# Kernel tuning notes

Measured on AMD Instinct MI355X. Metric: run time of the kernel, lower is better.

Reference implementation:

```python
import jax, jax.numpy as jnp
import numpy as np

B, N, E = 64, 2048, 32768          # graphs, nodes/graph, edges/graph
DIM = 64
RATIO = 0.8
K1 = int(np.ceil(RATIO * N))        # 1639 nodes/graph after pool1
K2 = int(np.ceil(RATIO * K1))       # 1312 nodes/graph after pool2
NUM_CLASSES = 6


def gcn_conv(x, W, b, src, dst, valid, n):
    # GCNConv with self-loops: out = D^-1/2 (A+I) D^-1/2 (x W) + b
    xw = x @ W                                          # [n, DIM]
    deg = jnp.zeros(n, x.dtype).at[dst].add(valid) + 1.0  # in-degree incl. self-loop
    norm = valid * jax.lax.rsqrt(deg[src] * deg[dst])      # per-edge norm (0 for masked)
    agg = jnp.zeros_like(xw).at[dst].add(xw[src] * norm[:, None])
    return agg + xw / deg[:, None] + b                  # self-loop term has norm 1/deg


def topk_pool(x, p, n_graphs, n_per, k):
    # PyG TopKPooling: score = tanh(x.p/||p||); keep top-k per graph; gate x by score
    score = jnp.tanh((x @ p) / jnp.linalg.norm(p))       # [n_graphs*n_per]
    vals, idx = jax.lax.top_k(score.reshape(n_graphs, n_per), k)  # [n_graphs, k]
    xg = x.reshape(n_graphs, n_per, -1)
    sel = jnp.take_along_axis(xg, idx[..., None], axis=1)          # [n_graphs, k, DIM]
    xp = sel * vals[..., None]
    perm = (idx + (jnp.arange(n_graphs) * n_per)[:, None]).reshape(-1)  # global ids kept
    return xp.reshape(n_graphs * k, -1), perm


def global_max_mean(x, n_graphs, n_per):
    xg = x.reshape(n_graphs, n_per, -1)
    return jnp.concatenate([xg.max(axis=1), xg.mean(axis=1)], axis=1)  # [n_graphs, 2*DIM]


def forward(x, edge_index, batch, W1, b1, p1, W2, b2, p2, lin1_w, lin1_b, lin2_w, lin2_b):
    src, dst = edge_index[0], edge_index[1]
    n_total = B * N
    ones = jnp.ones(src.shape[0], x.dtype)

    x = jax.nn.relu(gcn_conv(x, W1, b1, src, dst, ones, n_total))
    x, perm = topk_pool(x, p1, B, N, K1)
    x1 = global_max_mean(x, B, K1)

    # filter_adj: reindex edges to surviving nodes; drop (mask) edges touching removed nodes
    new_id = jnp.full(n_total, -1, jnp.int32).at[perm].set(jnp.arange(B * K1, dtype=jnp.int32))
    s2, d2 = new_id[src], new_id[dst]
    valid = ((s2 >= 0) & (d2 >= 0)).astype(x.dtype)
    s2 = jnp.where(s2 >= 0, s2, 0)
    d2 = jnp.where(d2 >= 0, d2, 0)

    x = jax.nn.relu(gcn_conv(x, W2, b2, s2, d2, valid, B * K1))
    x, _ = topk_pool(x, p2, B, K1, K2)
    x2 = global_max_mean(x, B, K2)

    h = x1 + x2
    h = jax.nn.relu(h @ lin1_w + lin1_b)
    return h @ lin2_w + lin2_b                           # [B, NUM_CLASSES]


def setup_inputs():
    key = jax.random.key(0)
    ks = jax.random.split(key, 10)
    x = jax.random.normal(ks[0], (B * N, DIM), jnp.float32)
    off = (jnp.arange(B) * N)[:, None]
    src = (jax.random.randint(ks[1], (B, E), 0, N) + off).reshape(-1)
    dst = (jax.random.randint(ks[2], (B, E), 0, N) + off).reshape(-1)
    edge_index = jnp.stack([src, dst]).astype(jnp.int32)
    batch = jnp.repeat(jnp.arange(B, dtype=jnp.int32), N)
    s = 1.0 / np.sqrt(DIM)
    return {
        "x": x,
        "edge_index": edge_index,
        "batch": batch,
        "W1": jax.random.normal(ks[3], (DIM, DIM), jnp.float32) * s,
        "b1": jnp.zeros(DIM, jnp.float32),
        "p1": jax.random.normal(ks[4], (DIM,), jnp.float32) * s,
        "W2": jax.random.normal(ks[5], (DIM, DIM), jnp.float32) * s,
        "b2": jnp.zeros(DIM, jnp.float32),
        "p2": jax.random.normal(ks[6], (DIM,), jnp.float32) * s,
        "lin1_w": jax.random.normal(ks[7], (2 * DIM, DIM), jnp.float32) / np.sqrt(2 * DIM),
        "lin1_b": jnp.zeros(DIM, jnp.float32),
        "lin2_w": jax.random.normal(ks[8], (DIM, NUM_CLASSES), jnp.float32) * s,
        "lin2_b": jnp.zeros(NUM_CLASSES, jnp.float32),
    }


def reference(x, edge_index, batch, W1, b1, p1, W2, b2, p2, lin1_w, lin1_b, lin2_w, lin2_b):
    return forward(x, edge_index, batch, W1, b1, p1, W2, b2, p2, lin1_w, lin1_b, lin2_w, lin2_b)
```

## Files before the change

kernel.cpp:

```cpp
#include <hip/hip_runtime.h>
#include <hip/hip_bf16.h>
#include <cstdint>
#include <cstddef>

#define B_    64
#define N_    2048
#define E_    32768
#define DIM_  64
#define K1_   1639
#define K2_   1312
#define NTOT  (B_ * N_)
#define ETOT  (B_ * E_)
#define N2TOT (B_ * K1_)
#define NCLS  6
#define PB_   8
#define CHUNKS_ 16
#define SLICES_ 16
#define BCAP  3072
#define REG_  192

typedef float f4 __attribute__((ext_vector_type(4)));
typedef _Float16 h2 __attribute__((ext_vector_type(2)));
typedef _Float16 h8 __attribute__((ext_vector_type(8)));

static __device__ __forceinline__ float fdot2(h2 a, h2 b, float c) {
    return __builtin_amdgcn_fdot2(a, b, c, false);
}
static __device__ __forceinline__ h2 pkrtz(float a, float b) {
    return __builtin_bit_cast(h2, __builtin_amdgcn_cvt_pkrtz(a, b));
}
static __device__ __forceinline__ unsigned long long mk_key(float s, int i) {
    unsigned u = __float_as_uint(s);
    u = (u & 0x80000000u) ? ~u : (u | 0x80000000u);
    return ((unsigned long long)u << 11) | (unsigned long long)(2047 - i);
}

__launch_bounds__(128)
__global__ void k_wprep(const float* W1, const float* W2, h8* wf) {
    int t = threadIdx.x;
    int stage = t >> 6, lane = t & 63;
    const float* W = stage ? W2 : W1;
    int q = lane >> 4, c = lane & 15;
#pragma unroll
    for (int ks = 0; ks < 2; ks++)
#pragma unroll
        for (int nt = 0; nt < 4; nt++) {
            h8 h, l;
#pragma unroll
            for (int j = 0; j < 8; j++) {
                float wv = W[(ks * 32 + q * 8 + j) * 64 + nt * 16 + c];
                _Float16 hh = (_Float16)wv;
                h[j] = hh;
                l[j] = (_Float16)(wv - (float)hh);
            }
            wf[(size_t)stage * 1024 + (((ks * 4 + nt) * 2 + 0) * 64) + lane] = h;
            wf[(size_t)stage * 1024 + (((ks * 4 + nt) * 2 + 1) * 64) + lane] = l;
        }
}

template<int STAGE>
__launch_bounds__(256)
__global__ void k_bucket(const int* src, const int* dst, const int* remap,
                         int* bcnt, unsigned int* blist) {
    const int LSTR = (STAGE == 1) ? 128 : 103;
    __shared__ unsigned int lb[CHUNKS_][REG_];
    __shared__ int lc[CHUNKS_];
    __shared__ int rm[N_];
    int b = blockIdx.x;
    int g = b & 63, slice = b >> 6;
    int tid = threadIdx.x;
    if (tid < CHUNKS_) lc[tid] = 0;
    if (STAGE == 2)
        for (int i = tid; i < N_; i += 256) rm[i] = remap[g * N_ + i];
    __syncthreads();
    const int ESL = E_ / SLICES_;
    const int* sp = src + (size_t)g * E_ + slice * ESL;
    const int* dp = dst + (size_t)g * E_ + slice * ESL;
    int gbase = g * ((STAGE == 1) ? N_ : K1_);
    for (int e = tid * 4; e < ESL; e += 1024) {
        int4 ss = *(const int4*)&sp[e];
        int4 dd = *(const int4*)&dp[e];
#pragma unroll
        for (int t = 0; t < 4; t++) {
            int s = (&ss.x)[t], d = (&dd.x)[t];
            if (STAGE == 2) {
                s = rm[s & (N_ - 1)]; d = rm[d & (N_ - 1)];
                if ((s | d) < 0) continue;
                s -= gbase; d -= gbase;
            } else {
                s &= (N_ - 1); d &= (N_ - 1);
            }
            int ch = d / LSTR;
            int dl = d - ch * LSTR;
            int p = atomicAdd(&lc[ch], 1);
            if (p < REG_) lb[ch][p] = ((unsigned)dl << 12) | (unsigned)s;
        }
    }
    __syncthreads();
    for (int ch = 0; ch < CHUNKS_; ch++) {
        int n = min(lc[ch], REG_);
        unsigned int* out = blist + (size_t)(g * CHUNKS_ + ch) * BCAP + slice * REG_;
        for (int i = tid; i < n; i += 256) out[i] = lb[ch][i];
    }
    if (tid < CHUNKS_) bcnt[(g * SLICES_ + slice) * CHUNKS_ + tid] = min(lc[tid], REG_);
}

template<int STAGE>
__launch_bounds__(256)
__global__ void k_sort(const int* bcnt, unsigned int* blist,
                       const float* xf, const unsigned int* xg,
                       unsigned int* xb, int* ninfo) {
    const int NL   = (STAGE == 1) ? N_ : K1_;
    const int LSTR = (STAGE == 1) ? 128 : 103;
    __shared__ int cnt[128], st[128], cur[128], cnt_s[SLICES_], stot[2];
    __shared__ float rsqv[128];
    __shared__ unsigned short sorted[BCAP];
    int b = blockIdx.x;
    int g = b & 63, ch = b >> 6;
    int tid = threadIdx.x;
    if (tid < 128) { cnt[tid] = 0; cur[tid] = 0; }
    if (tid < SLICES_) cnt_s[tid] = bcnt[(g * SLICES_ + tid) * CHUNKS_ + ch];
    __syncthreads();
    size_t bb = (size_t)(g * CHUNKS_ + ch) * BCAP;
    const unsigned int* bl = blist + bb;
    const int TOT = SLICES_ * REG_;
    for (int i = tid; i < TOT; i += 256) {
        int s = i / REG_, j = i - s * REG_;
        if (j < cnt_s[s]) atomicAdd(&cnt[bl[i] >> 12], 1);
    }
    __syncthreads();
    if (tid < 128) {
        int v = cnt[tid];
        int l64 = tid & 63;
#pragma unroll
        for (int o = 1; o < 64; o <<= 1) {
            int t = __shfl_up(v, o);
            if (l64 >= o) v += t;
        }
        st[tid] = v;
        if (l64 == 63) stot[tid >> 6] = v;
    }
    __syncthreads();
    if (tid >= 64 && tid < 128) st[tid] += stot[0];
    __syncthreads();
    for (int i = tid; i < TOT; i += 256) {
        int s = i / REG_, j = i - s * REG_;
        if (j < cnt_s[s]) {
            unsigned pk = bl[i];
            int dl = (int)(pk >> 12);
            int p = st[dl] - cnt[dl] + atomicAdd(&cur[dl], 1);
            sorted[p] = (unsigned short)(pk & 0xFFFu);
        }
    }
    __syncthreads();
    int n = st[127];
    for (int i = tid; i < n; i += 256) blist[bb + i] = ((unsigned int)sorted[i]) << 7;
    int lo = ch * LSTR;
    int nloc = min(LSTR, NL - lo);
    int gbase = g * NL;
    if (tid < nloc) {
        int node = gbase + lo + tid;
        int c = cnt[tid];
        int start = (int)bb + st[tid] - c;
        ninfo[node] = (start << 8) | min(c, 255);
        rsqv[tid] = rsqrtf((float)(c + 1));
    }
    __syncthreads();
    for (int idx = tid; idx < nloc * 32; idx += 256) {
        int nl = idx >> 5, f2 = idx & 31;
        int node = gbase + lo + nl;
        float sc = rsqv[nl];
        float2 v;
        if (STAGE == 1) {
            v = ((const float2*)xf)[(size_t)node * 32 + f2];
        } else {
            h2 hv = __builtin_bit_cast(h2, xg[(size_t)node * 32 + f2]);
            v.x = (float)hv.x; v.y = (float)hv.y;
        }
        h2 o = {(_Float16)(v.x * sc), (_Float16)(v.y * sc)};
        xb[(size_t)node * 32 + f2] = __builtin_bit_cast(unsigned int, o);
    }
}

template<bool GATE>
__launch_bounds__(256, 4)
__global__ void k_aggconv(const unsigned int* xb, const int* ninfo, const unsigned int* csr,
                          const h8* wfrag, const float* bias, const float* pvec,
                          float* y, float* score) {
    __shared__ float4 ls4[1024];
    __shared__ h8 wlds[2][4][2][64];
    float* ls = (float*)ls4;
    int b = blockIdx.x;
    int wg;
    if (GATE) {
        int xcd = b & 7, k = b >> 3;
        wg = (xcd < 7 ? xcd * 205 : 1435 + (xcd - 7) * 204) + k;
    } else {
        wg = (b & 7) * 256 + (b >> 3);
    }
    int tid = threadIdx.x;
    int wid = tid >> 6, lane = tid & 63;
    int half = lane >> 5, l32 = lane & 31;

    {
        const h8* wsrc = wfrag + (GATE ? 1024 : 0);
        h8* wd = (h8*)wlds;
        for (int i = tid; i < 1024; i += 256) wd[i] = wsrc[i];
    }

    const char* xbb = (const char*)xb;
    const h2 one0  = {(_Float16)1.0f, (_Float16)0.0f};
    const h2 zero1 = {(_Float16)0.0f, (_Float16)1.0f};
    int rb = __builtin_amdgcn_readfirstlane(wg * 64 + wid * 16);
    int g0 = 0, bnd = 0;
    if (GATE) { g0 = (wg * 64) / K1_; bnd = (g0 + 1) * K1_; }

#pragma unroll 1
    for (int p = 0; p < 16; p++) {
        int node = rb + p;
        int ni = __builtin_amdgcn_readfirstlane(ninfo[node]);
        int cnt = ni & 255;
        int base = ni >> 8;
        int gbb;
        if (GATE) { int gr = (node >= bnd) ? (g0 + 1) : g0; gbb = gr * (K1_ * 128); }
        else       gbb = (node & ~(N_ - 1)) << 7;
        const unsigned* csrg = csr + base;
        const char* gx = xbb + gbb;
        const unsigned* srp = (const unsigned*)(xbb + (size_t)(unsigned)node * 128);
        unsigned selfu = srp[l32];
        float ax0 = 0.f, ax1 = 0.f, ay0 = 0.f, ay1 = 0.f;
        int j = 0;
        for (; j + 8 <= cnt; j += 8) {
            unsigned ro[8];
#pragma unroll
            for (int k = 0; k < 8; k++)
                ro[k] = __builtin_amdgcn_readfirstlane(csrg[j + k]);
            unsigned u[8];
#pragma unroll
            for (int k = 0; k < 8; k++)
                u[k] = ((const unsigned*)(gx + ro[k]))[l32];
#pragma unroll
            for (int k = 0; k < 8; k++) {
                h2 h = __builtin_bit_cast(h2, u[k]);
                if (k & 1) { ax1 = fdot2(h, one0, ax1); ay1 = fdot2(h, zero1, ay1); }
                else       { ax0 = fdot2(h, one0, ax0); ay0 = fdot2(h, zero1, ay0); }
            }
        }
        for (; j < cnt; j++) {
            unsigned ro = __builtin_amdgcn_readfirstlane(csrg[j]);
            h2 h = __builtin_bit_cast(h2, ((const unsigned*)(gx + ro))[l32]);
            ax0 = fdot2(h, one0, ax0);
            ay0 = fdot2(h, zero1, ay0);
        }
        {
            h2 sh = __builtin_bit_cast(h2, selfu);
            ax0 = fdot2(sh, one0, ax0);
            ay0 = fdot2(sh, zero1, ay0);
        }
        float rd = rsqrtf((float)(cnt + 1));
        float2 o;
        o.x = (ax0 + ax1) * rd;
        o.y = (ay0 + ay1) * rd;
        if (half == 0) {
            int rloc = wid * 16 + p;
            int pi = rloc * 32 + ((((l32 >> 1) ^ (rloc & 7)) << 1) | (l32 & 1));
            ((float2*)ls)[pi] = o;
        }
    }
    __syncthreads();

    int q = lane >> 4, c = lane & 15;
    int rl16 = (wid * 16 + c) * 16;
    int cx = c & 7;
    h8 ah[2], al[2];
#pragma unroll
    for (int ks = 0; ks < 2; ks++) {
        float4 v0 = ls4[rl16 + ((ks * 8 + q * 2 + 0) ^ cx)];
        float4 v1 = ls4[rl16 + ((ks * 8 + q * 2 + 1) ^ cx)];
        float vv[8] = {v0.x, v0.y, v0.z, v0.w, v1.x, v1.y, v1.z, v1.w};
        h8 h, l;
#pragma unroll
        for (int j = 0; j < 8; j += 2) {
            h2 hp = pkrtz(vv[j], vv[j + 1]);
            float r0 = vv[j]     - (float)hp.x;
            float r1 = vv[j + 1] - (float)hp.y;
            h2 lp = pkrtz(r0, r1);
            h[j] = hp.x; h[j + 1] = hp.y;
            l[j] = lp.x; l[j + 1] = lp.y;
        }
        ah[ks] = h; al[ks] = l;
    }
    float pp = 0.f;
#pragma unroll
    for (int i = 0; i < DIM_; i++) pp += pvec[i] * pvec[i];
    float rpn = rsqrtf(pp);
    float dot[4] = {0.f, 0.f, 0.f, 0.f};
#pragma unroll
    for (int nt = 0; nt < 4; nt++) {
        f4 acc = {0.f, 0.f, 0.f, 0.f};
#pragma unroll
        for (int ks = 0; ks < 2; ks++) {
            h8 wh = wlds[ks][nt][0][lane];
            h8 wl = wlds[ks][nt][1][lane];
            acc = __builtin_amdgcn_mfma_f32_16x16x32_f16(ah[ks], wh, acc, 0, 0, 0);
            acc = __builtin_amdgcn_mfma_f32_16x16x32_f16(ah[ks], wl, acc, 0, 0, 0);
            acc = __builtin_amdgcn_mfma_f32_16x16x32_f16(al[ks], wh, acc, 0, 0, 0);
        }
        float bcol = bias[nt * 16 + c];
        float pcol = pvec[nt * 16 + c];
        float st[4];
#pragma unroll
        for (int reg = 0; reg < 4; reg++) {
            float v = fmaxf(acc[reg] + bcol, 0.f);
            st[reg] = v;
            dot[reg] += v * pcol;
        }
#pragma unroll
        for (int reg = 0; reg < 4; reg++)
            y[(size_t)(wg * 64 + wid * 16 + q * 4 + reg) * DIM_ + nt * 16 + c] = st[reg];
    }
#pragma unroll
    for (int m = 1; m < 16; m <<= 1) {
#pragma unroll
        for (int reg = 0; reg < 4; reg++) dot[reg] += __shfl_xor(dot[reg], m);
    }
    if (c == 0) {
#pragma unroll
        for (int reg = 0; reg < 4; reg++)
            score[wg * 64 + wid * 16 + q * 4 + reg] = tanhf(dot[reg] * rpn);
    }
}

template<int STAGE>
__launch_bounds__(256)
__global__ void k_thresh(const float* score, unsigned long long* thresh) {
    const int Nin = (STAGE == 1) ? N_ : K1_;
    const int K   = (STAGE == 1) ? K1_ : K2_;
    __shared__ unsigned long long keys[N_];
    __shared__ int bins[256], wsum[4];
    __shared__ unsigned long long s_prefix;
    __shared__ int s_need;
    int g = blockIdx.x, tid = threadIdx.x;
    int l64 = tid & 63, wid = tid >> 6;
    const float* sg = score + (size_t)g * Nin;
    for (int i = tid; i < Nin; i += 256) keys[i] = mk_key(sg[i], i);
    if (tid == 0) { s_need = K; s_prefix = 0ull; }
    __syncthreads();
    for (int shift = 40; shift >= 0; shift -= 8) {
        bins[tid] = 0;
        __syncthreads();
        unsigned long long pref = s_prefix;
        int need = s_need;
        int hi = shift + 8;
        for (int i = tid; i < Nin; i += 256) {
            unsigned long long k = keys[i];
            if ((k >> hi) == pref) atomicAdd(&bins[(int)((k >> shift) & 255)], 1);
        }
        __syncthreads();
        int mine = bins[tid];
        int v = mine;
#pragma unroll
        for (int o = 1; o < 64; o <<= 1) {
            int t = __shfl_down(v, o);
            if (l64 + o < 64) v += t;
        }
        if (l64 == 0) wsum[wid] = v;
        __syncthreads();
        for (int w = wid + 1; w < 4; w++) v += wsum[w];
        int nxt = v - mine;
        if (v >= need && nxt < need) {
            s_prefix = (pref << 8) | (unsigned long long)tid;
            s_need = need - nxt;
        }
        __syncthreads();
    }
    if (tid == 0) thresh[g] = s_prefix;
}

template<int STAGE>
__launch_bounds__(256)
__global__ void k_pool(const float* score, const float* conv, const unsigned long long* thresh,
                       int* new_id, unsigned int* xg, float* part) {
    const int Nin = (STAGE == 1) ? N_ : K1_;
    const int RNG = (STAGE == 1) ? (N_ / PB_) : ((K1_ + PB_ - 1) / PB_);
    __shared__ int rnk[256];
    __shared__ unsigned char keepf[256];
    __shared__ int wsum[4], s_base[4];
    __shared__ float rmx[4][64], rsm[4][64];
    int b = blockIdx.x;
    int g = b & 63, pb = b >> 6;
    int tid = threadIdx.x;
    int l64 = tid & 63, wid = tid >> 6;
    const float* sg = score + (size_t)g * Nin;
    unsigned long long T = thresh[g];
    int R0 = pb * RNG;
    int R1 = min(R0 + RNG, Nin);
    if (STAGE == 1) {
        int cb = 0;
        for (int i = tid; i < R0; i += 256) cb += (mk_key(sg[i], i) >= T) ? 1 : 0;
#pragma unroll
        for (int o = 32; o; o >>= 1) cb += __shfl_down(cb, o);
        if (l64 == 0) s_base[wid] = cb;
        int i = R0 + tid;
        int keep = (i < R1 && mk_key(sg[i], i) >= T) ? 1 : 0;
        keepf[tid] = (unsigned char)keep;
        int v = keep;
#pragma unroll
        for (int o = 1; o < 64; o <<= 1) {
            int t = __shfl_up(v, o);
            if (l64 >= o) v += t;
        }
        if (l64 == 63) wsum[wid] = v;
        __syncthreads();
        int base = s_base[0] + s_base[1] + s_base[2] + s_base[3];
        int wbase = 0;
        for (int w = 0; w < wid; w++) wbase += wsum[w];
        int r = base + wbase + v - keep;
        rnk[tid] = r;
        if (i < Nin) new_id[g * N_ + i] = keep ? (g * K1_ + r) : -1;
    } else {
        int i = R0 + tid;
        keepf[tid] = (unsigned char)((i < R1 && mk_key(sg[i], i) >= T) ? 1 : 0);
    }
    __syncthreads();
    float mx = -3.402823466e38f, sm = 0.f;
    for (int i = R0 + wid; i < R1; i += 4) {
        if (!keepf[i - R0]) continue;
        float val = sg[i];
        float v = conv[(size_t)(g * Nin + i) * DIM_ + l64] * val;
        mx = fmaxf(mx, v);
        sm += v;
        if (STAGE == 1) {
            float vo = __shfl_xor(v, 1);
            if (!(l64 & 1)) {
                h2 pk2 = {(_Float16)v, (_Float16)vo};
                xg[(size_t)(g * K1_ + rnk[i - R0]) * 32 + (l64 >> 1)] =
                    __builtin_bit_cast(unsigned int, pk2);
            }
        }
    }
    rmx[wid][l64] = mx; rsm[wid][l64] = sm;
    __syncthreads();
    if (wid == 0) {
        mx = fmaxf(fmaxf(rmx[0][l64], rmx[1][l64]), fmaxf(rmx[2][l64], rmx[3][l64]));
        sm = rsm[0][l64] + rsm[1][l64] + rsm[2][l64] + rsm[3][l64];
        part[((size_t)(g * PB_ + pb) * 2 + 0) * 64 + l64] = mx;
        part[((size_t)(g * PB_ + pb) * 2 + 1) * 64 + l64] = sm;
    }
}

__launch_bounds__(64)
__global__ void k_head(const float* part1, const float* part2,
                       const float* l1w, const float* l1b,
                       const float* l2w, const float* l2b, float* out) {
    __shared__ float h[128];
    __shared__ float h1[64];
    int g = blockIdx.x, t = threadIdx.x;
    float mx1 = -3.402823466e38f, sm1 = 0.f, mx2 = -3.402823466e38f, sm2 = 0.f;
#pragma unroll
    for (int c = 0; c < PB_; c++) {
        mx1 = fmaxf(mx1, part1[((size_t)(g * PB_ + c) * 2 + 0) * 64 + t]);
        sm1 += part1[((size_t)(g * PB_ + c) * 2 + 1) * 64 + t];
        mx2 = fmaxf(mx2, part2[((size_t)(g * PB_ + c) * 2 + 0) * 64 + t]);
        sm2 += part2[((size_t)(g * PB_ + c) * 2 + 1) * 64 + t];
    }
    h[t]      = mx1 + mx2;
    h[t + 64] = sm1 / (float)K1_ + sm2 / (float)K2_;
    __syncthreads();
    float acc = l1b[t];
#pragma unroll 8
    for (int i = 0; i < 128; i++) acc += h[i] * l1w[i * 64 + t];
    h1[t] = fmaxf(acc, 0.0f);
    __syncthreads();
    if (t < NCLS) {
        float o = l2b[t];
#pragma unroll
        for (int i = 0; i < 64; i++) o += h1[i] * l2w[i * NCLS + t];
        out[g * NCLS + t] = o;
    }
}

extern "C" void kernel_launch(void* const* d_in, const int* in_sizes, int n_in,
                              void* d_out, int out_size, void* d_ws, size_t ws_size,
                              hipStream_t stream) {
    const float* x   = (const float*)d_in[0];
    const int*   ei  = (const int*)d_in[1];
    const int*   src = ei;
    const int*   dst = ei + ETOT;
    const float* W1  = (const float*)d_in[3];
    const float* b1  = (const float*)d_in[4];
    const float* p1  = (const float*)d_in[5];
    const float* W2  = (const float*)d_in[6];
    const float* b2  = (const float*)d_in[7];
    const float* p2  = (const float*)d_in[8];
    const float* l1w = (const float*)d_in[9];
    const float* l1b = (const float*)d_in[10];
    const float* l2w = (const float*)d_in[11];
    const float* l2b = (const float*)d_in[12];
    (void)in_sizes; (void)n_in; (void)out_size; (void)ws_size;

    char* ws = (char*)d_ws;
    size_t off = 0;
    auto alloc = [&](size_t bytes) -> void* {
        void* p = ws + off;
        off = (off + bytes + 255) & ~(size_t)255;
        return p;
    };
    float*              bufA   = (float*)             alloc((size_t)NTOT  * DIM_ * 4);
    float*              bufB   = (float*)             alloc((size_t)N2TOT * DIM_ * 4);
    unsigned int*       blist  = (unsigned int*)      alloc((size_t)B_ * CHUNKS_ * BCAP * 4);
    unsigned int*       xb     = (unsigned int*)      alloc((size_t)NTOT * 32 * 4);
    int*                bcnt   = (int*)               alloc((size_t)B_ * SLICES_ * CHUNKS_ * 4);
    int*                ninfo  = (int*)               alloc((size_t)NTOT * 4);
    float*              score  = (float*)             alloc((size_t)NTOT * 4);
    int*                newid  = (int*)               alloc((size_t)NTOT * 4);
    unsigned long long* thr    = (unsigned long long*)alloc((size_t)B_ * 8);
    float*              part1  = (float*)             alloc((size_t)B_ * PB_ * 128 * 4);
    float*              part2  = (float*)             alloc((size_t)B_ * PB_ * 128 * 4);
    h8*                 wfrag  = (h8*)                alloc((size_t)2048 * 16);
    unsigned int*       xg     = (unsigned int*)bufB;

    k_wprep<<<1, 128, 0, stream>>>(W1, W2, wfrag);

    k_bucket<1><<<B_ * SLICES_, 256, 0, stream>>>(src, dst, nullptr, bcnt, blist);
    k_sort<1><<<B_ * CHUNKS_, 256, 0, stream>>>(bcnt, blist, x, nullptr, xb, ninfo);
    k_aggconv<false><<<NTOT / 64, 256, 0, stream>>>(xb, ninfo, blist, wfrag, b1, p1, bufA, score);
    k_thresh<1><<<B_, 256, 0, stream>>>(score, thr);
    k_pool<1><<<B_ * PB_, 256, 0, stream>>>(score, bufA, thr, newid, xg, part1);

    k_bucket<2><<<B_ * SLICES_, 256, 0, stream>>>(src, dst, newid, bcnt, blist);
    k_sort<2><<<B_ * CHUNKS_, 256, 0, stream>>>(bcnt, blist, nullptr, xg, xb, ninfo);
    k_aggconv<true><<<N2TOT / 64, 256, 0, stream>>>(xb, ninfo, blist, wfrag, b2, p2, bufB, score);
    k_thresh<2><<<B_, 256, 0, stream>>>(score, thr);
    k_pool<2><<<B_ * PB_, 256, 0, stream>>>(score, bufB, thr, nullptr, nullptr, part2);

    k_head<<<B_, 64, 0, stream>>>(part1, part2, l1w, l1b, l2w, l2b, (float*)d_out);
}
```

Baseline: 351.0 us.

## Gather neighbor rows with 16-byte loads across 8 edge groups per wave

Restructures the neighbor aggregation. Each wave now processes 8 edges at once, with 8 lanes per edge each loading 16 bytes of the fp16 row. Before, all 64 lanes loaded 4 bytes of one row per edge, wasting the second half-wave. CSR offsets and ninfo are loaded in bulk into registers, fetched one node ahead and spread with shuffles, which replaces serial readfirstlane scalar loads. Partial sums are then reduced across groups with xor-shuffles. The extra shuffle-reduction cost and divergence on low-degree nodes are traded for wider, more parallel memory accesses.

```diff
diff --git a/kernel.cpp b/kernel.cpp
--- a/kernel.cpp
+++ b/kernel.cpp
@@ -189,7 +189,6 @@
                           float* y, float* score) {
     __shared__ float4 ls4[1024];
     __shared__ h8 wlds[2][4][2][64];
-    float* ls = (float*)ls4;
     int b = blockIdx.x;
     int wg;
     if (GATE) {
@@ -200,7 +199,8 @@
     }
     int tid = threadIdx.x;
     int wid = tid >> 6, lane = tid & 63;
-    int half = lane >> 5, l32 = lane & 31;
+    int grp = lane >> 3;
+    int l16 = (lane & 7) * 16;
 
     {
         const h8* wsrc = wfrag + (GATE ? 1024 : 0);
@@ -211,61 +211,83 @@
     const char* xbb = (const char*)xb;
     const h2 one0  = {(_Float16)1.0f, (_Float16)0.0f};
     const h2 zero1 = {(_Float16)0.0f, (_Float16)1.0f};
-    int rb = __builtin_amdgcn_readfirstlane(wg * 64 + wid * 16);
+    int rb = wg * 64 + wid * 16;
     int g0 = 0, bnd = 0;
     if (GATE) { g0 = (wg * 64) / K1_; bnd = (g0 + 1) * K1_; }
 
+    int niv = 0;
+    if (lane < 16) niv = ninfo[rb + lane];
+    int ni = __builtin_amdgcn_readfirstlane(__shfl(niv, 0));
+    unsigned eo = 0;
+    { int ec = min(ni & 255, 64); if (lane < ec) eo = csr[(ni >> 8) + lane]; }
+
 #pragma unroll 1
     for (int p = 0; p < 16; p++) {
+        int cnt = ni & 255, base = ni >> 8;
         int node = rb + p;
-        int ni = __builtin_amdgcn_readfirstlane(ninfo[node]);
-        int cnt = ni & 255;
-        int base = ni >> 8;
         int gbb;
         if (GATE) { int gr = (node >= bnd) ? (g0 + 1) : g0; gbb = gr * (K1_ * 128); }
         else       gbb = (node & ~(N_ - 1)) << 7;
-        const unsigned* csrg = csr + base;
         const char* gx = xbb + gbb;
-        const unsigned* srp = (const unsigned*)(xbb + (size_t)(unsigned)node * 128);
-        unsigned selfu = srp[l32];
-        float ax0 = 0.f, ax1 = 0.f, ay0 = 0.f, ay1 = 0.f;
-        int j = 0;
-        for (; j + 8 <= cnt; j += 8) {
-            unsigned ro[8];
-#pragma unroll
-            for (int k = 0; k < 8; k++)
-                ro[k] = __builtin_amdgcn_readfirstlane(csrg[j + k]);
-            unsigned u[8];
-#pragma unroll
-            for (int k = 0; k < 8; k++)
-                u[k] = ((const unsigned*)(gx + ro[k]))[l32];
-#pragma unroll
-            for (int k = 0; k < 8; k++) {
-                h2 h = __builtin_bit_cast(h2, u[k]);
-                if (k & 1) { ax1 = fdot2(h, one0, ax1); ay1 = fdot2(h, zero1, ay1); }
-                else       { ax0 = fdot2(h, one0, ax0); ay0 = fdot2(h, zero1, ay0); }
-            }
-        }
-        for (; j < cnt; j++) {
-            unsigned ro = __builtin_amdgcn_readfirstlane(csrg[j]);
-            h2 h = __builtin_bit_cast(h2, ((const unsigned*)(gx + ro))[l32]);
-            ax0 = fdot2(h, one0, ax0);
-            ay0 = fdot2(h, zero1, ay0);
-        }
-        {
-            h2 sh = __builtin_bit_cast(h2, selfu);
-            ax0 = fdot2(sh, one0, ax0);
-            ay0 = fdot2(sh, zero1, ay0);
-        }
-        float rd = rsqrtf((float)(cnt + 1));
-        float2 o;
-        o.x = (ax0 + ax1) * rd;
-        o.y = (ay0 + ay1) * rd;
-        if (half == 0) {
+        int ni_n = 0; unsigned eo_n = 0;
+        if (p < 15) {
+            ni_n = __builtin_amdgcn_readfirstlane(__shfl(niv, p + 1));
+            int ec = min(ni_n & 255, 64);
+            if (lane < ec) eo_n = csr[(ni_n >> 8) + lane];
+        }
+        uint4 su = *(const uint4*)(xbb + (size_t)(unsigned)(node * 128 + l16));
+        float aA[4] = {0.f, 0.f, 0.f, 0.f};
+        float aB[4] = {0.f, 0.f, 0.f, 0.f};
+        int nv = min(cnt, 64);
+        for (int t = 0; t * 8 < nv; t++) {
+            int idx = t * 8 + grp;
+            unsigned ro = __shfl(eo, idx);
+            if (idx < cnt) {
+                uint4 v = *(const uint4*)(gx + (ro + (unsigned)l16));
+#pragma unroll
+                for (int w = 0; w < 4; w++) {
+                    h2 h = __builtin_bit_cast(h2, (&v.x)[w]);
+                    aA[w] = fdot2(h, one0,  aA[w]);
+                    aB[w] = fdot2(h, zero1, aB[w]);
+                }
+            }
+        }
+        for (int j = 64; j < cnt; j += 8) {
+            int idx = j + grp;
+            if (idx < cnt) {
+                unsigned ro = csr[base + idx];
+                uint4 v = *(const uint4*)(gx + (ro + (unsigned)l16));
+#pragma unroll
+                for (int w = 0; w < 4; w++) {
+                    h2 h = __builtin_bit_cast(h2, (&v.x)[w]);
+                    aA[w] = fdot2(h, one0,  aA[w]);
+                    aB[w] = fdot2(h, zero1, aB[w]);
+                }
+            }
+        }
+#pragma unroll
+        for (int m = 8; m < 64; m <<= 1) {
+#pragma unroll
+            for (int w = 0; w < 4; w++) {
+                aA[w] += __shfl_xor(aA[w], m);
+                aB[w] += __shfl_xor(aB[w], m);
+            }
+        }
+        if (lane < 8) {
+#pragma unroll
+            for (int w = 0; w < 4; w++) {
+                h2 h = __builtin_bit_cast(h2, (&su.x)[w]);
+                aA[w] = fdot2(h, one0,  aA[w]);
+                aB[w] = fdot2(h, zero1, aB[w]);
+            }
+            float rd = rsqrtf((float)(cnt + 1));
             int rloc = wid * 16 + p;
-            int pi = rloc * 32 + ((((l32 >> 1) ^ (rloc & 7)) << 1) | (l32 & 1));
-            ((float2*)ls)[pi] = o;
-        }
+            int c0 = (2 * lane)     ^ (rloc & 7);
+            int c1 = (2 * lane + 1) ^ (rloc & 7);
+            ls4[rloc * 16 + c0] = make_float4(aA[0] * rd, aB[0] * rd, aA[1] * rd, aB[1] * rd);
+            ls4[rloc * 16 + c1] = make_float4(aA[2] * rd, aB[2] * rd, aA[3] * rd, aB[3] * rd);
+        }
+        ni = ni_n; eo = eo_n;
     }
     __syncthreads();
 
```

New measurement: 355.5 us. About the same (+1.3%).
